# Performance work log

Measured on AMD Instinct MI355X. Metric: run time of the kernel, lower is better.

The kernel has to match this reference:

```python
import jax, jax.numpy as jnp
import numpy as np

D = 128; H = 8; L = 16; W = 32768; NN = 50000; T = 2; FH = 384  # FH = multiple_of-rounded 2/3*4*D
EPS = 1e-5


def rmsnorm(x, w):
    return x * jax.lax.rsqrt(jnp.mean(x * x, axis=-1, keepdims=True) + EPS) * w


def gru_dir(xi, Wh, bh, reverse):
    # xi: [L, W, 3D] precomputed input-gate activations (torch gate order r,z,n)
    def step(h, xt):
        g = h @ Wh.T + bh
        xr, xz, xn = jnp.split(xt, 3, -1)
        hr, hz, hn = jnp.split(g, 3, -1)
        r = jax.nn.sigmoid(xr + hr)
        z = jax.nn.sigmoid(xz + hz)
        n = jnp.tanh(xn + r * hn)
        hnew = (1.0 - z) * n + z * h
        return hnew, hnew
    h0 = jnp.zeros((xi.shape[1], Wh.shape[1]), xi.dtype)
    _, ys = jax.lax.scan(step, h0, xi, reverse=reverse)
    return ys  # [L, W, D]


def setup_inputs():
    key = jax.random.key(0)
    ks = jax.random.split(key, 24)
    rn = lambda i, shape, s=0.02: jax.random.normal(ks[i], shape, jnp.float32) * s
    z = lambda *s: jnp.zeros(s, jnp.float32)
    return {
        'x': jax.random.normal(ks[0], (W, L, D), jnp.float32),
        'walk_nodes': jax.random.randint(ks[1], (W, L), 0, NN, jnp.int32),
        'num_nodes': NN,
        'gru_norm_w': jnp.ones((D,), jnp.float32),
        'wi_f': rn(2, (3 * D, D)), 'wh_f': rn(3, (3 * D, D)), 'bi_f': z(3 * D), 'bh_f': z(3 * D),
        'wi_b': rn(4, (3 * D, D)), 'wh_b': rn(5, (3 * D, D)), 'bi_b': z(3 * D), 'bh_b': z(3 * D),
        'gru_out_w': rn(6, (D, 2 * D)),
        'ffn_norm_w': jnp.ones((D,), jnp.float32),
        'ffn_w1': rn(7, (FH, D)), 'ffn_w2': rn(8, (D, FH)), 'ffn_w3': rn(9, (FH, D)),
        'logit_w': rn(10, (H, D)), 'logit_b': z(H),
        'to_node_w': rn(11, (D, D)), 'to_node_b': z(D),
        'from_node_w': rn(12, (D, D)), 'from_node_b': z(D),
        'head_w1': rn(13, (128, D)), 'head_b1': z(128),
        'head_w2': rn(14, (128, 128)), 'head_b2': z(128),
        'head_w3': rn(15, (1, 128)), 'head_b3': z(1),
    }


def _forward(x, gru_norm_w, wi_f, wh_f, bi_f, bh_f, wi_b, wh_b, bi_b, bh_b,
             gru_out_w, ffn_norm_w, ffn_w1, ffn_w2, ffn_w3,
             logit_w, logit_b, to_node_w, to_node_b, from_node_w, from_node_b,
             head_w1, head_b1, head_w2, head_b2, head_w3, head_b3,
             walk_nodes, num_nodes):
    seg = walk_nodes.reshape(-1)  # [W*L] node ids
    Dh = D // H
    node_emb = None
    for _ in range(T):  # parameter-tied refinements
        # BidirectionalGRU block
        h = rmsnorm(x, gru_norm_w)
        xi_f = (h @ wi_f.T + bi_f).transpose(1, 0, 2)  # [L,W,3D]
        xi_b = (h @ wi_b.T + bi_b).transpose(1, 0, 2)
        yf = gru_dir(xi_f, wh_f, bh_f, False)
        yb = gru_dir(xi_b, wh_b, bh_b, True)
        y = jnp.concatenate([yf, yb], -1).transpose(1, 0, 2)  # [W,L,2D]
        x = x + y @ gru_out_w.T
        hf = rmsnorm(x, ffn_norm_w)
        x = x + (jax.nn.silu(hf @ ffn_w1.T) * (hf @ ffn_w3.T)) @ ffn_w2.T
        # attention scatter: segment softmax over node visits, multi-head
        flat = x.reshape(-1, D)  # [W*L, D]
        logits = flat @ logit_w.T + logit_b  # [W*L, H]
        m = jax.ops.segment_max(logits, seg, num_segments=num_nodes)
        m = jnp.where(jnp.isfinite(m), m, 0.0)
        e = jnp.exp(logits - m[seg])
        denom = jax.ops.segment_sum(e, seg, num_segments=num_nodes)
        attn = e / (denom[seg] + 1e-9)  # [W*L, H]
        v = (flat @ to_node_w.T + to_node_b).reshape(-1, H, Dh)
        weighted = (attn[:, :, None] * v).reshape(-1, D)
        node_emb = jax.ops.segment_sum(weighted, seg, num_segments=num_nodes)  # [NN, D]
        back = node_emb @ from_node_w.T + from_node_b
        x = x + back[seg].reshape(x.shape)  # additive refinement
    # scoring head MLP on node embeddings
    h1 = jax.nn.relu(node_emb @ head_w1.T + head_b1)
    h2 = jax.nn.relu(h1 @ head_w2.T + head_b2)
    return h2 @ head_w3.T + head_b3  # [NN, 1]


def reference(x, walk_nodes, num_nodes, gru_norm_w, wi_f, wh_f, bi_f, bh_f, wi_b, wh_b, bi_b, bh_b,
              gru_out_w, ffn_norm_w, ffn_w1, ffn_w2, ffn_w3,
              logit_w, logit_b, to_node_w, to_node_b, from_node_w, from_node_b,
              head_w1, head_b1, head_w2, head_b2, head_w3, head_b3):
    return _forward(x, gru_norm_w, wi_f, wh_f, bi_f, bh_f, wi_b, wh_b, bi_b, bh_b,
                    gru_out_w, ffn_norm_w, ffn_w1, ffn_w2, ffn_w3,
                    logit_w, logit_b, to_node_w, to_node_b, from_node_w, from_node_b,
                    head_w1, head_b1, head_w2, head_b2, head_w3, head_b3,
                    walk_nodes, num_nodes)
```

## Files before the change

kernel.cpp:

```cpp
#include <hip/hip_runtime.h>
#include <hip/hip_bf16.h>

#define WN 32768
#define LN 16
#define DN 128
#define WLN (WN * LN)
#define NNODES 50000
#define FHN 384

typedef __attribute__((ext_vector_type(8))) short short8;
typedef __attribute__((ext_vector_type(4))) float float4v;
typedef __hip_bfloat16 bf16;

__device__ __forceinline__ unsigned fenc(float f) {
  unsigned u = __float_as_uint(f);
  return (u & 0x80000000u) ? ~u : (u | 0x80000000u);
}
__device__ __forceinline__ float fdec(unsigned u) {
  unsigned v = (u & 0x80000000u) ? (u & 0x7FFFFFFFu) : ~u;
  return __uint_as_float(v);
}
__device__ __forceinline__ float sigm(float x) {
  return __builtin_amdgcn_rcpf(1.f + __expf(-x));
}
__device__ __forceinline__ float ftanh(float x) {
  return 1.f - 2.f * __builtin_amdgcn_rcpf(1.f + __expf(2.f * x));
}

__global__ __launch_bounds__(256) void wcat2_k(const float* __restrict__ wi,
                                               const float* __restrict__ wh,
                                               bf16* __restrict__ W) {
  int idx = blockIdx.x * 256 + threadIdx.x;
  int n2 = idx >> 8, k2 = idx & 255;
  float v;
  if (n2 < 256)      v = (k2 < 128) ? wi[n2 * 128 + k2] : wh[n2 * 128 + (k2 - 128)];
  else if (n2 < 384) v = (k2 < 128) ? wi[n2 * 128 + k2] : 0.f;
  else               v = (k2 < 128) ? 0.f : wh[(n2 - 128) * 128 + (k2 - 128)];
  W[idx] = (bf16)v;
}

__global__ __launch_bounds__(256) void conv2d_k(const float* __restrict__ src, int ld,
                                                bf16* __restrict__ dst, int cols, int total) {
  int idx = blockIdx.x * 256 + threadIdx.x;
  if (idx >= total) return;
  int r = idx / cols, c = idx - r * cols;
  dst[idx] = (bf16)src[(size_t)r * ld + c];
}

__global__ __launch_bounds__(256) void hist_k(const int* __restrict__ seg,
                                              unsigned* __restrict__ cnt) {
  long i = (long)blockIdx.x * 256 + threadIdx.x;
  atomicAdd(&cnt[seg[i]], 1u);
}

__global__ __launch_bounds__(1024) void scan_k(const unsigned* __restrict__ cnt,
                                               unsigned* __restrict__ off) {
  __shared__ unsigned sums[1024];
  const int tid = threadIdx.x;
  const int CH = (NNODES + 1023) / 1024;
  const int base = tid * CH;
  unsigned s = 0;
  for (int j = 0; j < CH; ++j) {
    int p = base + j;
    if (p < NNODES) s += cnt[p];
  }
  sums[tid] = s;
  __syncthreads();
  for (int o = 1; o < 1024; o <<= 1) {
    unsigned t = (tid >= o) ? sums[tid - o] : 0u;
    __syncthreads();
    sums[tid] += t;
    __syncthreads();
  }
  unsigned run = (tid > 0) ? sums[tid - 1] : 0u;
  for (int j = 0; j < CH; ++j) {
    int p = base + j;
    if (p < NNODES) { off[p] = run; run += cnt[p]; }
  }
  if (tid == 1023) off[NNODES] = sums[1023];
}

__global__ __launch_bounds__(256) void fill_k(const int* __restrict__ seg,
                                              unsigned* __restrict__ cursor,
                                              int* __restrict__ idx) {
  long i = (long)blockIdx.x * 256 + threadIdx.x;
  unsigned p = atomicAdd(&cursor[seg[i]], 1u);
  idx[p] = (int)i;
}

__global__ __launch_bounds__(256) void rmsnorm_bf16_k(const float* __restrict__ X,
                                                      const float* __restrict__ w,
                                                      bf16* __restrict__ out) {
  long row = (long)blockIdx.x * 4 + (threadIdx.x >> 6);
  int lane = threadIdx.x & 63;
  const float* x = X + row * 128;
  float v0 = x[lane], v1 = x[lane + 64];
  float ss = v0 * v0 + v1 * v1;
#pragma unroll
  for (int off = 32; off > 0; off >>= 1) ss += __shfl_down(ss, off);
  ss = __shfl(ss, 0);
  float r = rsqrtf(ss * (1.f / 128.f) + 1e-5f);
  out[row * 128 + lane] = (bf16)(v0 * r * w[lane]);
  out[row * 128 + lane + 64] = (bf16)(v1 * r * w[lane + 64]);
}

__global__ __launch_bounds__(256) void rmsnorm_gather_k(float* __restrict__ X,
                                                        const float* __restrict__ back,
                                                        const int* __restrict__ seg,
                                                        const float* __restrict__ w,
                                                        bf16* __restrict__ out) {
  long row = (long)blockIdx.x * 4 + (threadIdx.x >> 6);
  int lane = threadIdx.x & 63;
  int s = seg[row];
  float v0 = X[row * 128 + lane] + back[(long)s * 128 + lane];
  float v1 = X[row * 128 + lane + 64] + back[(long)s * 128 + lane + 64];
  X[row * 128 + lane] = v0;
  X[row * 128 + lane + 64] = v1;
  float ss = v0 * v0 + v1 * v1;
#pragma unroll
  for (int off = 32; off > 0; off >>= 1) ss += __shfl_down(ss, off);
  ss = __shfl(ss, 0);
  float r = rsqrtf(ss * (1.f / 128.f) + 1e-5f);
  out[row * 128 + lane] = (bf16)(v0 * r * w[lane]);
  out[row * 128 + lane + 64] = (bf16)(v1 * r * w[lane + 64]);
}

__global__ __launch_bounds__(512, 2) void gru_seq_k(const bf16* __restrict__ hbase,
                                                    bf16* __restrict__ yhist,
                                                    const bf16* __restrict__ W,
                                                    const float* __restrict__ bi,
                                                    const float* __restrict__ bh,
                                                    int reverse) {
  __shared__ __attribute__((aligned(16))) bf16 Ac[64][280];
  __shared__ __attribute__((aligned(16))) bf16 Bst[512][40];
  const int tid = threadIdx.x;
  const int w = tid >> 6, lane = tid & 63;
  const int c = lane & 15, qd = lane >> 4;
  const long rb = (long)blockIdx.x * 64;

  short8 breg[4][8];
#pragma unroll
  for (int kc = 0; kc < 8; ++kc) {
#pragma unroll
    for (int i = 0; i < 8; i++) {
      int q = tid + i * 512;
      int row = q >> 3, kq = (q & 7) * 4;
      *(ushort4*)&Bst[row][kq] = *(const ushort4*)(W + (size_t)row * 256 + kc * 32 + kq);
    }
    __syncthreads();
#pragma unroll
    for (int j = 0; j < 4; j++) {
      if ((j == 2 && kc >= 4) || (j == 3 && kc < 4)) continue;
      breg[j][kc] = *(const short8*)&Bst[(w + 8 * j) * 16 + c][qd * 8];
    }
    __syncthreads();
  }

  const int d = w * 16 + c;
  const float bR  = bi[d] + bh[d];
  const float bZ  = bi[128 + d] + bh[128 + d];
  const float bXN = bi[256 + d];
  const float bHN = bh[256 + d];

#pragma unroll
  for (int i = 0; i < 4; i++) {
    int q = tid + i * 512;
    int row = q >> 5, kq = (q & 31) * 4;
    *(ushort4*)&Ac[row][128 + kq] = make_ushort4(0, 0, 0, 0);
  }

  int lprev = 0;
  for (int t = 0; t < 16; ++t) {
    const int l = reverse ? (15 - t) : t;
#pragma unroll
    for (int i = 0; i < 4; i++) {
      int q = tid + i * 512;
      int row = q >> 5, kq = (q & 31) * 4;
      *(ushort4*)&Ac[row][kq] =
          *(const ushort4*)(hbase + ((rb + row) * 16 + l) * 128 + kq);
    }
    __syncthreads();
    if (t > 0) {
#pragma unroll
      for (int i = 0; i < 4; i++) {
        int q = tid + i * 512;
        int row = q >> 5, kq = (q & 31) * 4;
        *(ushort4*)(yhist + ((rb + row) * 16 + lprev) * 128 + kq) =
            *(const ushort4*)&Ac[row][128 + kq];
      }
    }
    float4v acc[4][4];
#pragma unroll
    for (int rt = 0; rt < 4; rt++)
#pragma unroll
      for (int j = 0; j < 4; j++) acc[rt][j] = (float4v)(0.f);
#pragma unroll
    for (int kc = 0; kc < 8; ++kc) {
      const int k0 = kc * 32;
      short8 af[4];
#pragma unroll
      for (int rt = 0; rt < 4; rt++)
        af[rt] = *(const short8*)&Ac[rt * 16 + c][k0 + qd * 8];
#pragma unroll
      for (int rt = 0; rt < 4; rt++) {
#pragma unroll
        for (int j = 0; j < 4; j++) {
          if ((j == 2 && kc >= 4) || (j == 3 && kc < 4)) continue;
          acc[rt][j] = __builtin_amdgcn_mfma_f32_16x16x32_bf16(af[rt], breg[j][kc], acc[rt][j], 0, 0, 0);
        }
      }
    }
    __syncthreads();
#pragma unroll
    for (int rt = 0; rt < 4; rt++) {
#pragma unroll
      for (int reg = 0; reg < 4; ++reg) {
        int row = rt * 16 + qd * 4 + reg;
        float r = sigm(acc[rt][0][reg] + bR);
        float z = sigm(acc[rt][1][reg] + bZ);
        float n = ftanh(acc[rt][2][reg] + bXN + r * (acc[rt][3][reg] + bHN));
        float hold = (float)Ac[row][128 + d];
        Ac[row][128 + d] = (bf16)((1.f - z) * n + z * hold);
      }
    }
    lprev = l;
  }
  __syncthreads();
#pragma unroll
  for (int i = 0; i < 4; i++) {
    int q = tid + i * 512;
    int row = q >> 5, kq = (q & 31) * 4;
    *(ushort4*)(yhist + ((rb + row) * 16 + lprev) * 128 + kq) =
        *(const ushort4*)&Ac[row][128 + kq];
  }
}

template <int EPI>
__global__ __launch_bounds__(256, 2) void mm_bf16_k(const bf16* __restrict__ A, int lda,
                                                    const bf16* __restrict__ B, int ldb,
                                                    float* __restrict__ C, int ldc, int K,
                                                    const float* __restrict__ nw,
                                                    bf16* __restrict__ hout) {
  __shared__ __attribute__((aligned(16))) bf16 As[64][40];
  __shared__ __attribute__((aligned(16))) bf16 Bs[128][40];
  const int tid = threadIdx.x;
  const int wave = tid >> 6, lane = tid & 63;
  const long rb = (long)blockIdx.x * 64;
  const int nb = blockIdx.y * 128;
  float4v acc[8];
#pragma unroll
  for (int i = 0; i < 8; i++) acc[i] = (float4v)(0.f);
  for (int k0 = 0; k0 < K; k0 += 32) {
#pragma unroll
    for (int i = 0; i < 2; i++) {
      int q = tid + i * 256;
      int row = q >> 3, kq = (q & 7) * 4;
      *(ushort4*)&As[row][kq] = *(const ushort4*)(A + (rb + row) * (size_t)lda + k0 + kq);
    }
#pragma unroll
    for (int i = 0; i < 4; i++) {
      int q = tid + i * 256;
      int row = q >> 3, kq = (q & 7) * 4;
      *(ushort4*)&Bs[row][kq] = *(const ushort4*)(B + (size_t)(nb + row) * ldb + k0 + kq);
    }
    __syncthreads();
    short8 af = *(const short8*)&As[wave * 16 + (lane & 15)][(lane >> 4) * 8];
#pragma unroll
    for (int ct = 0; ct < 8; ++ct) {
      short8 bf = *(const short8*)&Bs[ct * 16 + (lane & 15)][(lane >> 4) * 8];
      acc[ct] = __builtin_amdgcn_mfma_f32_16x16x32_bf16(af, bf, acc[ct], 0, 0, 0);
    }
    __syncthreads();
  }
  const int c = lane & 15, qd = lane >> 4;
  if (EPI == 3) {
#pragma unroll
    for (int reg = 0; reg < 4; ++reg) {
      long row = rb + wave * 16 + qd * 4 + reg;
      float v[8];
      float ssq = 0.f;
#pragma unroll
      for (int ct = 0; ct < 8; ++ct) {
        int n = ct * 16 + c;
        v[ct] = C[row * 128 + n] + acc[ct][reg];
        ssq += v[ct] * v[ct];
      }
      ssq += __shfl_xor(ssq, 1);
      ssq += __shfl_xor(ssq, 2);
      ssq += __shfl_xor(ssq, 4);
      ssq += __shfl_xor(ssq, 8);
      float rr = rsqrtf(ssq * (1.f / 128.f) + 1e-5f);
#pragma unroll
      for (int ct = 0; ct < 8; ++ct) {
        int n = ct * 16 + c;
        C[row * 128 + n] = v[ct];
        hout[row * 128 + n] = (bf16)(v[ct] * rr * nw[n]);
      }
    }
  } else {
#pragma unroll
    for (int ct = 0; ct < 8; ++ct) {
      int n = nb + ct * 16 + c;
#pragma unroll
      for (int reg = 0; reg < 4; ++reg) {
        long row = rb + wave * 16 + qd * 4 + reg;
        if (EPI == 2) C[row * ldc + n] += acc[ct][reg];
        else C[row * ldc + n] = acc[ct][reg];
      }
    }
  }
}

__global__ __launch_bounds__(256, 2) void tonode_mm_k(const float* __restrict__ A,
                                                      const bf16* __restrict__ B,
                                                      bf16* __restrict__ V) {
  __shared__ __attribute__((aligned(16))) bf16 As[64][40];
  __shared__ __attribute__((aligned(16))) bf16 Bs[128][40];
  const int tid = threadIdx.x;
  const int wave = tid >> 6, lane = tid & 63;
  const long rb = (long)blockIdx.x * 64;
  float4v acc[8];
#pragma unroll
  for (int i = 0; i < 8; i++) acc[i] = (float4v)(0.f);
  for (int k0 = 0; k0 < 128; k0 += 32) {
#pragma unroll
    for (int i = 0; i < 2; i++) {
      int q = tid + i * 256;
      int row = q >> 3, kq = (q & 7) * 4;
      float4 f = *(const float4*)(A + (rb + row) * 128 + k0 + kq);
      bf16 t4[4] = {(bf16)f.x, (bf16)f.y, (bf16)f.z, (bf16)f.w};
      *(ushort4*)&As[row][kq] = *(const ushort4*)t4;
    }
#pragma unroll
    for (int i = 0; i < 4; i++) {
      int q = tid + i * 256;
      int row = q >> 3, kq = (q & 7) * 4;
      *(ushort4*)&Bs[row][kq] = *(const ushort4*)(B + (size_t)row * 128 + k0 + kq);
    }
    __syncthreads();
    short8 af = *(const short8*)&As[wave * 16 + (lane & 15)][(lane >> 4) * 8];
#pragma unroll
    for (int ct = 0; ct < 8; ++ct) {
      short8 bf = *(const short8*)&Bs[ct * 16 + (lane & 15)][(lane >> 4) * 8];
      acc[ct] = __builtin_amdgcn_mfma_f32_16x16x32_bf16(af, bf, acc[ct], 0, 0, 0);
    }
    __syncthreads();
  }
  const int c = lane & 15, qd = lane >> 4;
#pragma unroll
  for (int ct = 0; ct < 8; ++ct) {
    int n = ct * 16 + c;
#pragma unroll
    for (int reg = 0; reg < 4; ++reg) {
      long row = rb + wave * 16 + qd * 4 + reg;
      V[row * 128 + n] = (bf16)acc[ct][reg];
    }
  }
}

__global__ __launch_bounds__(128) void gather_k(const bf16* __restrict__ V,
                                                const float* __restrict__ e,
                                                const float* __restrict__ denom,
                                                const float* __restrict__ bias,
                                                const unsigned* __restrict__ off,
                                                const int* __restrict__ idx,
                                                float* __restrict__ node_emb) {
  const int s = blockIdx.x;
  const int d = threadIdx.x;
  const int hh = d >> 4;
  const unsigned beg = off[s], end = off[s + 1];
  float accv = 0.f, accw = 0.f;
  for (unsigned p = beg; p < end; ++p) {
    long i = idx[p];
    float w = e[i * 8 + hh];
    accv = fmaf(w, (float)V[i * 128 + d], accv);
    accw += w;
  }
  float dn = denom[(long)s * 8 + hh] + 1e-9f;
  node_emb[(long)s * 128 + d] = (accv + accw * bias[d]) / dn;
}

__global__ __launch_bounds__(256, 2) void ffn_gate2_k(const bf16* __restrict__ A,
                                                      const bf16* __restrict__ W13,
                                                      bf16* __restrict__ U) {
  __shared__ __attribute__((aligned(16))) bf16 As[64][40];
  __shared__ __attribute__((aligned(16))) bf16 Bs[256][40];
  const int tid = threadIdx.x;
  const int wave = tid >> 6, lane = tid & 63;
  const long rb = (long)blockIdx.x * 64;
  const int nb = blockIdx.y * 128;
  float4v a1[8], a3[8];
#pragma unroll
  for (int i = 0; i < 8; i++) { a1[i] = (float4v)(0.f); a3[i] = (float4v)(0.f); }
  for (int k0 = 0; k0 < 128; k0 += 32) {
#pragma unroll
    for (int i = 0; i < 2; i++) {
      int q = tid + i * 256;
      int row = q >> 3, kq = (q & 7) * 4;
      *(ushort4*)&As[row][kq] = *(const ushort4*)(A + (rb + row) * 128 + k0 + kq);
    }
#pragma unroll
    for (int i = 0; i < 8; i++) {
      int q = tid + i * 256;
      int row = q >> 3, kq = (q & 7) * 4;
      int srcrow = (row < 128) ? (nb + row) : (384 + nb + row - 128);
      *(ushort4*)&Bs[row][kq] = *(const ushort4*)(W13 + (size_t)srcrow * 128 + k0 + kq);
    }
    __syncthreads();
    short8 af = *(const short8*)&As[wave * 16 + (lane & 15)][(lane >> 4) * 8];
#pragma unroll
    for (int ct = 0; ct < 8; ++ct) {
      short8 b1 = *(const short8*)&Bs[ct * 16 + (lane & 15)][(lane >> 4) * 8];
      a1[ct] = __builtin_amdgcn_mfma_f32_16x16x32_bf16(af, b1, a1[ct], 0, 0, 0);
      short8 b3 = *(const short8*)&Bs[128 + ct * 16 + (lane & 15)][(lane >> 4) * 8];
      a3[ct] = __builtin_amdgcn_mfma_f32_16x16x32_bf16(af, b3, a3[ct], 0, 0, 0);
    }
    __syncthreads();
  }
  const int c = lane & 15, qd = lane >> 4;
#pragma unroll
  for (int ct = 0; ct < 8; ++ct) {
    int d = nb + ct * 16 + c;
#pragma unroll
    for (int reg = 0; reg < 4; ++reg) {
      long row = rb + wave * 16 + qd * 4 + reg;
      float g = a1[ct][reg];
      U[row * 384 + d] = (bf16)(g * sigm(g) * a3[ct][reg]);
    }
  }
}

enum { EPI_STORE = 0, EPI_RELU = 1 };
template <int EPI>
__global__ __launch_bounds__(256) void gemm_k(const float* __restrict__ A, int lda,
                                              const float* __restrict__ B, int ldb,
                                              const float* __restrict__ bias,
                                              float* __restrict__ C, int ldc,
                                              int M, int N, int K) {
  __shared__ float As[16][68];
  __shared__ float Bs[16][68];
  const int tid = threadIdx.x;
  const int bm = blockIdx.x * 64;
  const int bn = blockIdx.y * 64;
  const int lm = tid >> 2;
  const int lk = (tid & 3) << 2;
  const int tm = (tid >> 4) << 2;
  const int tn = (tid & 15) << 2;
  float acc[4][4] = {};
  for (int k0 = 0; k0 < K; k0 += 16) {
    float4 av = make_float4(0.f, 0.f, 0.f, 0.f);
    if (bm + lm < M)
      av = *reinterpret_cast<const float4*>(A + (long)(bm + lm) * lda + k0 + lk);
    As[lk + 0][lm] = av.x; As[lk + 1][lm] = av.y; As[lk + 2][lm] = av.z; As[lk + 3][lm] = av.w;
    float4 bv = *reinterpret_cast<const float4*>(B + (long)(bn + lm) * ldb + k0 + lk);
    Bs[lk + 0][lm] = bv.x; Bs[lk + 1][lm] = bv.y; Bs[lk + 2][lm] = bv.z; Bs[lk + 3][lm] = bv.w;
    __syncthreads();
#pragma unroll
    for (int k = 0; k < 16; k++) {
      float a[4], b[4];
#pragma unroll
      for (int j = 0; j < 4; j++) { a[j] = As[k][tm + j]; b[j] = Bs[k][tn + j]; }
#pragma unroll
      for (int i = 0; i < 4; i++)
#pragma unroll
        for (int j = 0; j < 4; j++) acc[i][j] = fmaf(a[i], b[j], acc[i][j]);
    }
    __syncthreads();
  }
#pragma unroll
  for (int i = 0; i < 4; i++) {
    int gm = bm + tm + i;
    if (gm < M) {
      float* crow = C + (long)gm * ldc + bn;
#pragma unroll
      for (int j = 0; j < 4; j++) {
        float v = acc[i][j] + (bias ? bias[bn + tn + j] : 0.f);
        if (EPI == EPI_RELU) v = fmaxf(v, 0.f);
        crow[tn + j] = v;
      }
    }
  }
}

__global__ __launch_bounds__(256) void logits_k(const float* __restrict__ X,
                                                const float* __restrict__ LW,
                                                const float* __restrict__ LB,
                                                float* __restrict__ out) {
  __shared__ float w[1024];
  __shared__ float b[8];
  int tid = threadIdx.x;
  for (int i = tid; i < 1024; i += 256) w[i] = LW[i];
  if (tid < 8) b[tid] = LB[tid];
  __syncthreads();
  long r = (long)blockIdx.x * 32 + (tid >> 3);
  int hh = tid & 7;
  const float* x = X + r * 128;
  const float* wr = w + hh * 128;
  float s = 0.f;
#pragma unroll 16
  for (int k = 0; k < 128; k++) s = fmaf(x[k], wr[k], s);
  out[r * 8 + hh] = s + b[hh];
}

__global__ __launch_bounds__(256) void segmax_k(const float* __restrict__ logits,
                                                const int* __restrict__ seg,
                                                unsigned* __restrict__ menc) {
  long idx = (long)blockIdx.x * 256 + threadIdx.x;
  long i = idx >> 3;
  int hh = idx & 7;
  atomicMax(&menc[(long)seg[i] * 8 + hh], fenc(logits[idx]));
}

__global__ __launch_bounds__(256) void expdenom_k(float* __restrict__ e_or_logits,
                                                  const int* __restrict__ seg,
                                                  const unsigned* __restrict__ menc,
                                                  float* __restrict__ denom) {
  long idx = (long)blockIdx.x * 256 + threadIdx.x;
  long i = idx >> 3;
  int hh = idx & 7;
  int s = seg[i];
  float ev = expf(e_or_logits[idx] - fdec(menc[(long)s * 8 + hh]));
  e_or_logits[idx] = ev;
  atomicAdd(&denom[(long)s * 8 + hh], ev);
}

__global__ __launch_bounds__(256) void head3_k(const float* __restrict__ H2,
                                               const float* __restrict__ W3,
                                               const float* __restrict__ B3,
                                               float* __restrict__ out, int M) {
  int row = blockIdx.x * 4 + (threadIdx.x >> 6);
  int lane = threadIdx.x & 63;
  if (row >= M) return;
  const float* x = H2 + (long)row * 128;
  float s = x[lane] * W3[lane] + x[lane + 64] * W3[lane + 64];
#pragma unroll
  for (int off = 32; off > 0; off >>= 1) s += __shfl_down(s, off);
  if (lane == 0) out[row] = s + B3[0];
}

extern "C" void kernel_launch(void* const* d_in, const int* in_sizes, int n_in,
                              void* d_out, int out_size, void* d_ws, size_t ws_size,
                              hipStream_t stream) {
  (void)in_sizes; (void)n_in; (void)out_size; (void)ws_size;
  const float* in_x       = (const float*)d_in[0];
  const int*   seg        = (const int*)d_in[1];
  const float* gru_norm_w = (const float*)d_in[3];
  const float* wi_f       = (const float*)d_in[4];
  const float* wh_f       = (const float*)d_in[5];
  const float* bi_f       = (const float*)d_in[6];
  const float* bh_f       = (const float*)d_in[7];
  const float* wi_b       = (const float*)d_in[8];
  const float* wh_b       = (const float*)d_in[9];
  const float* bi_b       = (const float*)d_in[10];
  const float* bh_b       = (const float*)d_in[11];
  const float* gru_out_w  = (const float*)d_in[12];
  const float* ffn_norm_w = (const float*)d_in[13];
  const float* ffn_w1     = (const float*)d_in[14];
  const float* ffn_w2     = (const float*)d_in[15];
  const float* ffn_w3     = (const float*)d_in[16];
  const float* logit_w    = (const float*)d_in[17];
  const float* logit_b    = (const float*)d_in[18];
  const float* to_node_w  = (const float*)d_in[19];
  const float* to_node_b  = (const float*)d_in[20];
  const float* from_node_w= (const float*)d_in[21];
  const float* from_node_b= (const float*)d_in[22];
  const float* head_w1    = (const float*)d_in[23];
  const float* head_b1    = (const float*)d_in[24];
  const float* head_w2    = (const float*)d_in[25];
  const float* head_b2    = (const float*)d_in[26];
  const float* head_w3    = (const float*)d_in[27];
  const float* head_b3    = (const float*)d_in[28];
  float* out = (float*)d_out;

  float* ws = (float*)d_ws;
  size_t o = 0;
  auto alloc = [&](size_t n) { float* p = ws + o; o += (n + 63) & ~(size_t)63; return p; };
  float* xbuf = alloc((size_t)WLN * 128);
  bf16*  hb16 = (bf16*)alloc((size_t)WLN * 64);
  float* pool = alloc((size_t)WLN * 64);
  bf16* yhist = (bf16*)pool;
  bf16*     ub16   = (bf16*)pool;
  float*    ebuf   = pool + (size_t)65536 * 384 / 2;
  unsigned* menc   = (unsigned*)(ebuf + (size_t)WLN * 8);
  float*    denomb = (float*)(menc + (size_t)NNODES * 8);
  float* h1b = pool;
  float* h2b = pool + (size_t)NNODES * 128;
  bf16* vbuf = hb16;
  float* node_emb = alloc((size_t)NNODES * 128);
  float* backb    = alloc((size_t)NNODES * 128);
  bf16* Wcat2_f = (bf16*)alloc(512 * 256 / 2);
  bf16* Wcat2_b = (bf16*)alloc(512 * 256 / 2);
  bf16* WoF     = (bf16*)alloc(128 * 128 / 2);
  bf16* WoB     = (bf16*)alloc(128 * 128 / 2);
  bf16* W13     = (bf16*)alloc(768 * 128 / 2);
  bf16* W2b     = (bf16*)alloc(128 * 384 / 2);
  bf16* Wtn     = (bf16*)alloc(128 * 128 / 2);
  unsigned* cntb = (unsigned*)alloc(NNODES);
  unsigned* offb = (unsigned*)alloc(NNODES + 1);
  unsigned* curb = (unsigned*)alloc(NNODES + 1);
  int*      idxb = (int*)alloc(WLN);

  hipLaunchKernelGGL(wcat2_k, dim3(512), dim3(256), 0, stream, wi_f, wh_f, Wcat2_f);
  hipLaunchKernelGGL(wcat2_k, dim3(512), dim3(256), 0, stream, wi_b, wh_b, Wcat2_b);
  hipLaunchKernelGGL(conv2d_k, dim3(64), dim3(256), 0, stream, gru_out_w, 256, WoF, 128, 128 * 128);
  hipLaunchKernelGGL(conv2d_k, dim3(64), dim3(256), 0, stream, gru_out_w + 128, 256, WoB, 128, 128 * 128);
  hipLaunchKernelGGL(conv2d_k, dim3(192), dim3(256), 0, stream, ffn_w1, 128, W13, 128, 384 * 128);
  hipLaunchKernelGGL(conv2d_k, dim3(192), dim3(256), 0, stream, ffn_w3, 128, W13 + 384 * 128, 128, 384 * 128);
  hipLaunchKernelGGL(conv2d_k, dim3(192), dim3(256), 0, stream, ffn_w2, 384, W2b, 384, 128 * 384);
  hipLaunchKernelGGL(conv2d_k, dim3(64), dim3(256), 0, stream, to_node_w, 128, Wtn, 128, 128 * 128);

  hipMemsetAsync(cntb, 0, (size_t)NNODES * 4, stream);
  hipLaunchKernelGGL(hist_k, dim3(WLN / 256), dim3(256), 0, stream, seg, cntb);
  hipLaunchKernelGGL(scan_k, dim3(1), dim3(1024), 0, stream, cntb, offb);
  hipMemcpyAsync(curb, offb, (size_t)NNODES * 4, hipMemcpyDeviceToDevice, stream);
  hipLaunchKernelGGL(fill_k, dim3(WLN / 256), dim3(256), 0, stream, seg, curb, idxb);

  hipMemcpyAsync(xbuf, in_x, (size_t)WLN * 128 * 4, hipMemcpyDeviceToDevice, stream);

  for (int it = 0; it < 2; ++it) {
    if (it == 0)
      hipLaunchKernelGGL(rmsnorm_bf16_k, dim3(WLN / 4), dim3(256), 0, stream, xbuf, gru_norm_w, hb16);
    else
      hipLaunchKernelGGL(rmsnorm_gather_k, dim3(WLN / 4), dim3(256), 0, stream, xbuf, backb, seg, gru_norm_w, hb16);
    hipLaunchKernelGGL(gru_seq_k, dim3(WN / 64), dim3(512), 0, stream,
                       hb16, yhist, Wcat2_f, bi_f, bh_f, 0);
    hipLaunchKernelGGL((mm_bf16_k<2>), dim3(WLN / 64, 1), dim3(256), 0, stream,
                       yhist, 128, WoF, 128, xbuf, 128, 128, (const float*)nullptr, (bf16*)nullptr);
    hipLaunchKernelGGL(gru_seq_k, dim3(WN / 64), dim3(512), 0, stream,
                       hb16, yhist, Wcat2_b, bi_b, bh_b, 1);
    hipLaunchKernelGGL((mm_bf16_k<3>), dim3(WLN / 64, 1), dim3(256), 0, stream,
                       yhist, 128, WoB, 128, xbuf, 128, 128, ffn_norm_w, hb16);

    for (int c = 0; c < 8; ++c) {
      const int CM = WLN / 8;
      hipLaunchKernelGGL(ffn_gate2_k, dim3(CM / 64, 3), dim3(256), 0, stream,
                         hb16 + (size_t)c * CM * 128, W13, ub16);
      hipLaunchKernelGGL((mm_bf16_k<2>), dim3(CM / 64, 1), dim3(256), 0, stream,
                         ub16, 384, W2b, 384, xbuf + (size_t)c * CM * 128, 128, 384,
                         (const float*)nullptr, (bf16*)nullptr);
    }

    hipLaunchKernelGGL(logits_k, dim3(WLN / 32), dim3(256), 0, stream, xbuf, logit_w, logit_b, ebuf);
    hipMemsetAsync(menc, 0, (size_t)NNODES * 8 * 4, stream);
    hipMemsetAsync(denomb, 0, (size_t)NNODES * 8 * 4, stream);
    hipLaunchKernelGGL(segmax_k, dim3(WLN * 8 / 256), dim3(256), 0, stream, ebuf, seg, menc);
    hipLaunchKernelGGL(expdenom_k, dim3(WLN * 8 / 256), dim3(256), 0, stream, ebuf, seg, menc, denomb);
    hipLaunchKernelGGL(tonode_mm_k, dim3(WLN / 64), dim3(256), 0, stream, xbuf, Wtn, vbuf);
    hipLaunchKernelGGL(gather_k, dim3(NNODES), dim3(128), 0, stream,
                       vbuf, ebuf, denomb, to_node_b, offb, idxb, node_emb);
    if (it == 0) {
      hipLaunchKernelGGL((gemm_k<EPI_STORE>), dim3((NNODES + 63) / 64, 2), dim3(256), 0, stream,
                         node_emb, 128, from_node_w, 128, from_node_b, backb, 128, NNODES, 128, 128);
    }
  }

  hipLaunchKernelGGL((gemm_k<EPI_RELU>), dim3((NNODES + 63) / 64, 2), dim3(256), 0, stream,
                     node_emb, 128, head_w1, 128, head_b1, h1b, 128, NNODES, 128, 128);
  hipLaunchKernelGGL((gemm_k<EPI_RELU>), dim3((NNODES + 63) / 64, 2), dim3(256), 0, stream,
                     h1b, 128, head_w2, 128, head_b2, h2b, 128, NNODES, 128, 128);
  hipLaunchKernelGGL(head3_k, dim3((NNODES + 3) / 4), dim3(256), 0, stream, h2b, head_w3, head_b3, out, NNODES);
}
```

Before: 4.260 ms.

## Restructure GRU scan: 128-row tiles, streamed weights, double-buffered inputs, register hidden state

The GRU recurrence kernel now handles 128 walks per block instead of 64 and no longer keeps the recurrent weights resident in registers. Weight fragments are streamed from global or L2 with one-step-ahead prefetch inside the k loop. The next timestep's input is loaded into a second LDS buffer during the gate epilogue. The previous hidden state is kept in fp32 registers rather than re-read from LDS. This cuts the grid in half and frees registers for larger accumulator tiles, but it reloads the weights every timestep, adds LDS use (three 128x136 buffers), and may reduce occupancy.

```diff
diff --git a/kernel.cpp b/kernel.cpp
--- a/kernel.cpp
+++ b/kernel.cpp
@@ -131,30 +131,18 @@
                                                     const float* __restrict__ bi,
                                                     const float* __restrict__ bh,
                                                     int reverse) {
-  __shared__ __attribute__((aligned(16))) bf16 Ac[64][280];
-  __shared__ __attribute__((aligned(16))) bf16 Bst[512][40];
+  __shared__ __attribute__((aligned(16))) bf16 X0[128][136];
+  __shared__ __attribute__((aligned(16))) bf16 X1[128][136];
+  __shared__ __attribute__((aligned(16))) bf16 Hs[128][136];
   const int tid = threadIdx.x;
   const int w = tid >> 6, lane = tid & 63;
   const int c = lane & 15, qd = lane >> 4;
-  const long rb = (long)blockIdx.x * 64;
-
-  short8 breg[4][8];
-#pragma unroll
-  for (int kc = 0; kc < 8; ++kc) {
-#pragma unroll
-    for (int i = 0; i < 8; i++) {
-      int q = tid + i * 512;
-      int row = q >> 3, kq = (q & 7) * 4;
-      *(ushort4*)&Bst[row][kq] = *(const ushort4*)(W + (size_t)row * 256 + kc * 32 + kq);
-    }
-    __syncthreads();
-#pragma unroll
-    for (int j = 0; j < 4; j++) {
-      if ((j == 2 && kc >= 4) || (j == 3 && kc < 4)) continue;
-      breg[j][kc] = *(const short8*)&Bst[(w + 8 * j) * 16 + c][qd * 8];
-    }
-    __syncthreads();
-  }
+  const long rb = (long)blockIdx.x * 128;
+
+  const size_t p0 = ((size_t)(w +  0) * 16 + c) * 256 + qd * 8;
+  const size_t p1 = ((size_t)(w +  8) * 16 + c) * 256 + qd * 8;
+  const size_t p2 = ((size_t)(w + 16) * 16 + c) * 256 + qd * 8;
+  const size_t p3 = ((size_t)(w + 24) * 16 + c) * 256 + qd * 8;
 
   const int d = w * 16 + c;
   const float bR  = bi[d] + bh[d];
@@ -162,76 +150,104 @@
   const float bXN = bi[256 + d];
   const float bHN = bh[256 + d];
 
-#pragma unroll
-  for (int i = 0; i < 4; i++) {
-    int q = tid + i * 512;
-    int row = q >> 5, kq = (q & 31) * 4;
-    *(ushort4*)&Ac[row][128 + kq] = make_ushort4(0, 0, 0, 0);
-  }
-
-  int lprev = 0;
-  for (int t = 0; t < 16; ++t) {
-    const int l = reverse ? (15 - t) : t;
+  const short8 zseed = {0, 0, 0, 0, 0, 0, 0, 0};
+  {
+    const int l0 = reverse ? 15 : 0;
 #pragma unroll
     for (int i = 0; i < 4; i++) {
       int q = tid + i * 512;
-      int row = q >> 5, kq = (q & 31) * 4;
-      *(ushort4*)&Ac[row][kq] =
-          *(const ushort4*)(hbase + ((rb + row) * 16 + l) * 128 + kq);
-    }
-    __syncthreads();
+      int row = q >> 4, kq = (q & 15) * 8;
+      *(short8*)&Hs[row][kq] = zseed;
+      *(short8*)&X0[row][kq] =
+          *(const short8*)(hbase + ((rb + row) * 16 + l0) * 128 + kq);
+    }
+  }
+  float hprev[8][4];
+#pragma unroll
+  for (int rt = 0; rt < 8; rt++)
+#pragma unroll
+    for (int r2 = 0; r2 < 4; r2++) hprev[rt][r2] = 0.f;
+  __syncthreads();
+
+  for (int t = 0; t < 16; ++t) {
+    const bf16 (*Xc)[136] = (t & 1) ? X1 : X0;
+    bf16 (*Xn)[136] = (t & 1) ? X0 : X1;
     if (t > 0) {
+      const int lp = reverse ? (16 - t) : (t - 1);
 #pragma unroll
       for (int i = 0; i < 4; i++) {
         int q = tid + i * 512;
-        int row = q >> 5, kq = (q & 31) * 4;
-        *(ushort4*)(yhist + ((rb + row) * 16 + lprev) * 128 + kq) =
-            *(const ushort4*)&Ac[row][128 + kq];
-      }
-    }
-    float4v acc[4][4];
-#pragma unroll
-    for (int rt = 0; rt < 4; rt++)
-#pragma unroll
-      for (int j = 0; j < 4; j++) acc[rt][j] = (float4v)(0.f);
+        int row = q >> 4, kq = (q & 15) * 8;
+        *(short8*)(yhist + ((rb + row) * 16 + lp) * 128 + kq) =
+            *(const short8*)&Hs[row][kq];
+      }
+    }
+    float4v acc[8][4];
+    short8 nb0 = *(const short8*)(W + p0);
+    short8 nb1 = *(const short8*)(W + p1);
+    short8 nb2 = *(const short8*)(W + p2);
 #pragma unroll
     for (int kc = 0; kc < 8; ++kc) {
-      const int k0 = kc * 32;
-      short8 af[4];
-#pragma unroll
-      for (int rt = 0; rt < 4; rt++)
-        af[rt] = *(const short8*)&Ac[rt * 16 + c][k0 + qd * 8];
-#pragma unroll
-      for (int rt = 0; rt < 4; rt++) {
-#pragma unroll
-        for (int j = 0; j < 4; j++) {
-          if ((j == 2 && kc >= 4) || (j == 3 && kc < 4)) continue;
-          acc[rt][j] = __builtin_amdgcn_mfma_f32_16x16x32_bf16(af[rt], breg[j][kc], acc[rt][j], 0, 0, 0);
-        }
-      }
-    }
-    __syncthreads();
-#pragma unroll
-    for (int rt = 0; rt < 4; rt++) {
+      short8 b0 = nb0, b1 = nb1, b2 = nb2;
+      if (kc < 7) {
+        const int kn = kc + 1;
+        nb0 = *(const short8*)(W + p0 + kn * 32);
+        nb1 = *(const short8*)(W + p1 + kn * 32);
+        nb2 = (kn < 4) ? *(const short8*)(W + p2 + kn * 32)
+                       : *(const short8*)(W + p3 + kn * 32);
+      }
+      const int col = (kc & 3) * 32 + qd * 8;
+      const bf16 (*Asrc)[136] = (kc < 4) ? Xc : (const bf16 (*)[136])Hs;
+#pragma unroll
+      for (int rt = 0; rt < 8; rt++) {
+        short8 af = *(const short8*)&Asrc[rt * 16 + c][col];
+        acc[rt][0] = __builtin_amdgcn_mfma_f32_16x16x32_bf16(
+            af, b0, (kc == 0) ? (float4v)(0.f) : acc[rt][0], 0, 0, 0);
+        acc[rt][1] = __builtin_amdgcn_mfma_f32_16x16x32_bf16(
+            af, b1, (kc == 0) ? (float4v)(0.f) : acc[rt][1], 0, 0, 0);
+        if (kc < 4)
+          acc[rt][2] = __builtin_amdgcn_mfma_f32_16x16x32_bf16(
+              af, b2, (kc == 0) ? (float4v)(0.f) : acc[rt][2], 0, 0, 0);
+        else
+          acc[rt][3] = __builtin_amdgcn_mfma_f32_16x16x32_bf16(
+              af, b2, (kc == 4) ? (float4v)(0.f) : acc[rt][3], 0, 0, 0);
+      }
+    }
+    __syncthreads();
+#pragma unroll
+    for (int rt = 0; rt < 8; rt++) {
 #pragma unroll
       for (int reg = 0; reg < 4; ++reg) {
         int row = rt * 16 + qd * 4 + reg;
         float r = sigm(acc[rt][0][reg] + bR);
         float z = sigm(acc[rt][1][reg] + bZ);
         float n = ftanh(acc[rt][2][reg] + bXN + r * (acc[rt][3][reg] + bHN));
-        float hold = (float)Ac[row][128 + d];
-        Ac[row][128 + d] = (bf16)((1.f - z) * n + z * hold);
-      }
-    }
-    lprev = l;
-  }
-  __syncthreads();
-#pragma unroll
-  for (int i = 0; i < 4; i++) {
-    int q = tid + i * 512;
-    int row = q >> 5, kq = (q & 31) * 4;
-    *(ushort4*)(yhist + ((rb + row) * 16 + lprev) * 128 + kq) =
-        *(const ushort4*)&Ac[row][128 + kq];
+        float hnew = (1.f - z) * n + z * hprev[rt][reg];
+        hprev[rt][reg] = hnew;
+        Hs[row][d] = (bf16)hnew;
+      }
+    }
+    if (t < 15) {
+      const int ln = reverse ? (14 - t) : (t + 1);
+#pragma unroll
+      for (int i = 0; i < 4; i++) {
+        int q = tid + i * 512;
+        int row = q >> 4, kq = (q & 15) * 8;
+        *(short8*)&Xn[row][kq] =
+            *(const short8*)(hbase + ((rb + row) * 16 + ln) * 128 + kq);
+      }
+    }
+    __syncthreads();
+  }
+  {
+    const int lp = reverse ? 0 : 15;
+#pragma unroll
+    for (int i = 0; i < 4; i++) {
+      int q = tid + i * 512;
+      int row = q >> 4, kq = (q & 15) * 8;
+      *(short8*)(yhist + ((rb + row) * 16 + lp) * 128 + kq) =
+          *(const short8*)&Hs[row][kq];
+    }
   }
 }
 
@@ -622,11 +638,11 @@
       hipLaunchKernelGGL(rmsnorm_bf16_k, dim3(WLN / 4), dim3(256), 0, stream, xbuf, gru_norm_w, hb16);
     else
       hipLaunchKernelGGL(rmsnorm_gather_k, dim3(WLN / 4), dim3(256), 0, stream, xbuf, backb, seg, gru_norm_w, hb16);
-    hipLaunchKernelGGL(gru_seq_k, dim3(WN / 64), dim3(512), 0, stream,
+    hipLaunchKernelGGL(gru_seq_k, dim3(WN / 128), dim3(512), 0, stream,
                        hb16, yhist, Wcat2_f, bi_f, bh_f, 0);
     hipLaunchKernelGGL((mm_bf16_k<2>), dim3(WLN / 64, 1), dim3(256), 0, stream,
                        yhist, 128, WoF, 128, xbuf, 128, 128, (const float*)nullptr, (bf16*)nullptr);
-    hipLaunchKernelGGL(gru_seq_k, dim3(WN / 64), dim3(512), 0, stream,
+    hipLaunchKernelGGL(gru_seq_k, dim3(WN / 128), dim3(512), 0, stream,
                        hb16, yhist, Wcat2_b, bi_b, bh_b, 1);
     hipLaunchKernelGGL((mm_bf16_k<3>), dim3(WLN / 64, 1), dim3(256), 0, stream,
                        yhist, 128, WoB, 128, xbuf, 128, 128, ffn_norm_w, hb16);
```

New measurement: 4.378 ms. +2.8%, slower.
